# Performance work log

Hardware: AMD Instinct MI355X
Metric: run time of the kernel (lower is better)

The kernel has to match this reference:

```python
import jax, jax.numpy as jnp
import numpy as np


def setup_inputs() -> dict:
    key = jax.random.key(0)
    k1, k2 = jax.random.split(key)
    B, S, D, T = 64, 512, 768, 384
    hidden_states = jax.random.normal(k1, (B, S, D), dtype=jnp.float32)
    # sorted per-row segment ids: each subtoken belongs to a token index in [0, T)
    segment_ids = jnp.sort(jax.random.randint(k2, (B, S), 0, T), axis=-1)
    return {"hidden_states": hidden_states, "segment_ids": segment_ids, "num_tokens": T}


def reference(hidden_states, segment_ids, num_tokens):
    # Segment-mean of subtoken embeddings into token embeddings.
    # Equivalent to the original running-mean loop:
    #   prev + (next - prev) / n_subtoken_per_token  == mean over the group.
    B, S, D = hidden_states.shape
    # flatten batch into segment ids so one segment_sum handles all sequences
    flat_ids = (segment_ids + jnp.arange(B, dtype=segment_ids.dtype)[:, None] * num_tokens).reshape(-1)
    sums = jax.ops.segment_sum(hidden_states.reshape(-1, D), flat_ids,
                               num_segments=B * num_tokens)  # [B*T, D]
    counts = jax.ops.segment_sum(jnp.ones((B * S,), dtype=hidden_states.dtype), flat_ids,
                                 num_segments=B * num_tokens)  # [B*T]
    # tokens with no subtokens stay zero (original initializes with zeros)
    means = sums / jnp.maximum(counts, 1.0)[:, None]
    return means.reshape(B, num_tokens, D)
```

## Files before the change

### kernel.cpp

```cpp
#include <hip/hip_runtime.h>


__global__ void __launch_bounds__(192) seg_mean_kernel(
    const float* __restrict__ hs,
    const int* __restrict__ seg,
    const int* __restrict__ num_tokens_p,
    float* __restrict__ out,
    int BS_total,
    int D) {
  const int T = num_tokens_p[0];
  const int BT = gridDim.x;
  const int S = (int)(((long long)BS_total * T) / BT);
  const int b = blockIdx.x / T;
  const int t = blockIdx.x - b * T;

  const int* __restrict__ row = seg + (size_t)b * S;

  int lo = 0, n = S;
  while (n > 0) {
    int half = n >> 1;
    int mid = lo + half;
    if (row[mid] < t) { lo = mid + 1; n -= half + 1; } else { n = half; }
  }
  int hi = lo; n = S - lo;
  while (n > 0) {
    int half = n >> 1;
    int mid = hi + half;
    if (row[mid] < t + 1) { hi = mid + 1; n -= half + 1; } else { n = half; }
  }
  const int cnt = hi - lo;

  const int d4 = threadIdx.x;
  const int rowstride4 = D >> 2;

  const float4* __restrict__ p =
      (const float4*)(hs + ((size_t)b * S + lo) * D) + d4;

  float4 acc = make_float4(0.f, 0.f, 0.f, 0.f);
  for (int s = 0; s < cnt; ++s) {
    float4 v = p[(size_t)s * rowstride4];
    acc.x += v.x; acc.y += v.y; acc.z += v.z; acc.w += v.w;
  }

  const float inv = (cnt > 0) ? (1.0f / (float)cnt) : 0.0f;
  float4 o = make_float4(acc.x * inv, acc.y * inv, acc.z * inv, acc.w * inv);

  ((float4*)(out + (size_t)blockIdx.x * D))[d4] = o;
}

extern "C" void kernel_launch(void* const* d_in, const int* in_sizes, int n_in,
                              void* d_out, int out_size, void* d_ws, size_t ws_size,
                              hipStream_t stream) {
  const float* hs = (const float*)d_in[0];
  const int* seg = (const int*)d_in[1];
  const int* num_tokens_p = (const int*)d_in[2];
  float* out = (float*)d_out;

  const int BS_total = in_sizes[1];
  const int D = in_sizes[0] / in_sizes[1];
  const int BT = out_size / D;

  dim3 grid(BT);
  dim3 block(D / 4);
  hipLaunchKernelGGL(seg_mean_kernel, grid, block, 0, stream,
                     hs, seg, num_tokens_p, out, BS_total, D);
}
```

Measured before the change: 181.1 us.

## Precompute per-token segment start offsets in a separate kernel instead of binary search

Adds a preliminary kernel that scans the sorted segment ids and writes a per-row table of token start offsets into workspace. The mean kernel then reads its start and end from this table instead of running two dependent binary searches over the segment row. This removes the serial global-memory load chains at block start, at the cost of an extra launch and a workspace dependency. The old search-based kernel is kept as a fallback when workspace is too small.

```diff
diff --git a/kernel.cpp b/kernel.cpp
--- a/kernel.cpp
+++ b/kernel.cpp
@@ -1,9 +1,30 @@
 #include <hip/hip_runtime.h>
 
 
+__global__ void bounds_kernel(const int* __restrict__ seg,
+                              const int* __restrict__ num_tokens_p,
+                              int* __restrict__ start,
+                              int BS_total,
+                              int BT) {
+  const int T = num_tokens_p[0];
+  const int B = BT / T;
+  const int S = BS_total / B;
+  int idx = blockIdx.x * blockDim.x + threadIdx.x;
+  if (idx >= BS_total) return;
+  const int b = idx / S;
+  const int s = idx - b * S;
+  const int cur = seg[idx];
+  const int prev = (s == 0) ? -1 : seg[idx - 1];
+  int* __restrict__ row = start + (size_t)b * (T + 1);
+  for (int t = prev + 1; t <= cur; ++t) row[t] = s;
+  if (s == S - 1) {
+    for (int t = cur + 1; t <= T; ++t) row[t] = S;
+  }
+}
+
 __global__ void __launch_bounds__(192) seg_mean_kernel(
     const float* __restrict__ hs,
-    const int* __restrict__ seg,
+    const int* __restrict__ start,
     const int* __restrict__ num_tokens_p,
     float* __restrict__ out,
     int BS_total,
@@ -14,20 +35,9 @@
   const int b = blockIdx.x / T;
   const int t = blockIdx.x - b * T;
 
-  const int* __restrict__ row = seg + (size_t)b * S;
-
-  int lo = 0, n = S;
-  while (n > 0) {
-    int half = n >> 1;
-    int mid = lo + half;
-    if (row[mid] < t) { lo = mid + 1; n -= half + 1; } else { n = half; }
-  }
-  int hi = lo; n = S - lo;
-  while (n > 0) {
-    int half = n >> 1;
-    int mid = hi + half;
-    if (row[mid] < t + 1) { hi = mid + 1; n -= half + 1; } else { n = half; }
-  }
+  const int* __restrict__ srow = start + (size_t)b * (T + 1) + t;
+  const int lo = srow[0];
+  const int hi = srow[1];
   const int cnt = hi - lo;
 
   const int d4 = threadIdx.x;
@@ -48,6 +58,49 @@
   ((float4*)(out + (size_t)blockIdx.x * D))[d4] = o;
 }
 
+__global__ void __launch_bounds__(192) seg_mean_search_kernel(
+    const float* __restrict__ hs,
+    const int* __restrict__ seg,
+    const int* __restrict__ num_tokens_p,
+    float* __restrict__ out,
+    int BS_total,
+    int D) {
+  const int T = num_tokens_p[0];
+  const int BT = gridDim.x;
+  const int S = (int)(((long long)BS_total * T) / BT);
+  const int b = blockIdx.x / T;
+  const int t = blockIdx.x - b * T;
+  const int* __restrict__ row = seg + (size_t)b * S;
+
+  int lo = 0, n = S;
+  while (n > 0) {
+    int half = n >> 1;
+    int mid = lo + half;
+    if (row[mid] < t) { lo = mid + 1; n -= half + 1; } else { n = half; }
+  }
+  int hi = lo; n = S - lo;
+  while (n > 0) {
+    int half = n >> 1;
+    int mid = hi + half;
+    if (row[mid] < t + 1) { hi = mid + 1; n -= half + 1; } else { n = half; }
+  }
+  const int cnt = hi - lo;
+
+  const int d4 = threadIdx.x;
+  const int rowstride4 = D >> 2;
+  const float4* __restrict__ p =
+      (const float4*)(hs + ((size_t)b * S + lo) * D) + d4;
+
+  float4 acc = make_float4(0.f, 0.f, 0.f, 0.f);
+  for (int s = 0; s < cnt; ++s) {
+    float4 v = p[(size_t)s * rowstride4];
+    acc.x += v.x; acc.y += v.y; acc.z += v.z; acc.w += v.w;
+  }
+  const float inv = (cnt > 0) ? (1.0f / (float)cnt) : 0.0f;
+  float4 o = make_float4(acc.x * inv, acc.y * inv, acc.z * inv, acc.w * inv);
+  ((float4*)(out + (size_t)blockIdx.x * D))[d4] = o;
+}
+
 extern "C" void kernel_launch(void* const* d_in, const int* in_sizes, int n_in,
                               void* d_out, int out_size, void* d_ws, size_t ws_size,
                               hipStream_t stream) {
@@ -60,8 +113,18 @@
   const int D = in_sizes[0] / in_sizes[1];
   const int BT = out_size / D;
 
-  dim3 grid(BT);
-  dim3 block(D / 4);
-  hipLaunchKernelGGL(seg_mean_kernel, grid, block, 0, stream,
-                     hs, seg, num_tokens_p, out, BS_total, D);
+  const size_t ws_needed = (size_t)4 * ((size_t)BT + (size_t)BS_total);
+
+  if (ws_size >= ws_needed) {
+    int* start = (int*)d_ws;
+    const int threads1 = 256;
+    const int grid1 = (BS_total + threads1 - 1) / threads1;
+    hipLaunchKernelGGL(bounds_kernel, dim3(grid1), dim3(threads1), 0, stream,
+                       seg, num_tokens_p, start, BS_total, BT);
+    hipLaunchKernelGGL(seg_mean_kernel, dim3(BT), dim3(D / 4), 0, stream,
+                       hs, start, num_tokens_p, out, BS_total, D);
+  } else {
+    hipLaunchKernelGGL(seg_mean_search_kernel, dim3(BT), dim3(D / 4), 0, stream,
+                       hs, seg, num_tokens_p, out, BS_total, D);
+  }
 }
```

After: 174.7 us. -3.5%, faster.

## Precompute segment boundary table and process several tokens per wavefront

Applied to the files above, without the earlier changes.

Adds a first kernel that scatters segment start offsets into a workspace table, replacing the per-block binary searches over segment ids. The main kernel then assigns four consecutive tokens to each 64-lane wavefront, with each lane accumulating several float4 chunks in registers. This removes the search latency and the 192-thread blocks. In exchange it adds a second kernel launch and fewer, longer-running waves, which may lower memory-level parallelism for a bandwidth-bound read of about 100MB.

```diff
diff --git a/kernel.cpp b/kernel.cpp
--- a/kernel.cpp
+++ b/kernel.cpp
@@ -1,51 +1,88 @@
 #include <hip/hip_runtime.h>
 
 
-__global__ void __launch_bounds__(192) seg_mean_kernel(
+#define TPW 4
+#define WPB 4
+#define TPB (TPW * WPB)
+
+__global__ void table_kernel(const int* __restrict__ seg,
+                             const int* __restrict__ num_tokens_p,
+                             int* __restrict__ table,
+                             int BS_total,
+                             int BT) {
+  const int T = num_tokens_p[0];
+  const int B = BT / T;
+  const int S = BS_total / B;
+  int s = blockIdx.x * blockDim.x + threadIdx.x;
+  if (s >= BS_total) return;
+  const int b = s / S;
+  const int cur = b * T + seg[s];
+  const int prev = (s == 0) ? -1 : ((s - 1) / S) * T + seg[s - 1];
+  for (int g = prev + 1; g <= cur; ++g) table[g] = s;
+  if (s == BS_total - 1) {
+    for (int g = cur + 1; g <= BT; ++g) table[g] = BS_total;
+  }
+}
+
+template <int NCH>
+__global__ __launch_bounds__(WPB * 64) void seg_mean_kernel(
     const float* __restrict__ hs,
-    const int* __restrict__ seg,
-    const int* __restrict__ num_tokens_p,
+    const int* __restrict__ table,
     float* __restrict__ out,
-    int BS_total,
-    int D) {
-  const int T = num_tokens_p[0];
-  const int BT = gridDim.x;
-  const int S = (int)(((long long)BS_total * T) / BT);
-  const int b = blockIdx.x / T;
-  const int t = blockIdx.x - b * T;
+    int BT,
+    int D4) {
+  const int lane = threadIdx.x & 63;
+  const int wid = threadIdx.x >> 6;
+  const int g0 = (blockIdx.x * WPB + wid) * TPW;
+  if (g0 >= BT) return;
+  const int n = min(TPW, BT - g0);
 
-  const int* __restrict__ row = seg + (size_t)b * S;
+  int bnd[TPW + 1];
+#pragma unroll
+  for (int i = 0; i <= TPW; ++i) bnd[i] = (i <= n) ? table[g0 + i] : 0;
 
-  int lo = 0, n = S;
-  while (n > 0) {
-    int half = n >> 1;
-    int mid = lo + half;
-    if (row[mid] < t) { lo = mid + 1; n -= half + 1; } else { n = half; }
+  const float4* __restrict__ hs4 = (const float4*)hs;
+  float4* __restrict__ out4 = (float4*)out;
+
+  int r = bnd[0];
+  for (int tok = 0; tok < n; ++tok) {
+    const int rend = bnd[tok + 1];
+    float4 acc[NCH];
+#pragma unroll
+    for (int c = 0; c < NCH; ++c) acc[c] = make_float4(0.f, 0.f, 0.f, 0.f);
+    for (; r < rend; ++r) {
+      const float4* __restrict__ p = hs4 + (size_t)r * D4 + lane;
+#pragma unroll
+      for (int c = 0; c < NCH; ++c) {
+        float4 v = p[c * 64];
+        acc[c].x += v.x; acc[c].y += v.y; acc[c].z += v.z; acc[c].w += v.w;
+      }
+    }
+    const int cnt = rend - bnd[tok];
+    const float inv = (cnt > 0) ? (1.0f / (float)cnt) : 0.0f;
+    float4* __restrict__ q = out4 + (size_t)(g0 + tok) * D4 + lane;
+#pragma unroll
+    for (int c = 0; c < NCH; ++c) {
+      q[c * 64] = make_float4(acc[c].x * inv, acc[c].y * inv,
+                              acc[c].z * inv, acc[c].w * inv);
+    }
   }
-  int hi = lo; n = S - lo;
-  while (n > 0) {
-    int half = n >> 1;
-    int mid = hi + half;
-    if (row[mid] < t + 1) { hi = mid + 1; n -= half + 1; } else { n = half; }
+}
+
+__global__ void seg_mean_fallback(const float* __restrict__ hs,
+                                  const int* __restrict__ table,
+                                  float* __restrict__ out,
+                                  int D) {
+  const int g = blockIdx.x;
+  const int lo = table[g];
+  const int hi = table[g + 1];
+  const int cnt = hi - lo;
+  const float inv = (cnt > 0) ? (1.0f / (float)cnt) : 0.0f;
+  for (int d = threadIdx.x; d < D; d += blockDim.x) {
+    float a = 0.f;
+    for (int r = lo; r < hi; ++r) a += hs[(size_t)r * D + d];
+    out[(size_t)g * D + d] = a * inv;
   }
-  const int cnt = hi - lo;
-
-  const int d4 = threadIdx.x;
-  const int rowstride4 = D >> 2;
-
-  const float4* __restrict__ p =
-      (const float4*)(hs + ((size_t)b * S + lo) * D) + d4;
-
-  float4 acc = make_float4(0.f, 0.f, 0.f, 0.f);
-  for (int s = 0; s < cnt; ++s) {
-    float4 v = p[(size_t)s * rowstride4];
-    acc.x += v.x; acc.y += v.y; acc.z += v.z; acc.w += v.w;
-  }
-
-  const float inv = (cnt > 0) ? (1.0f / (float)cnt) : 0.0f;
-  float4 o = make_float4(acc.x * inv, acc.y * inv, acc.z * inv, acc.w * inv);
-
-  ((float4*)(out + (size_t)blockIdx.x * D))[d4] = o;
 }
 
 extern "C" void kernel_launch(void* const* d_in, const int* in_sizes, int n_in,
@@ -60,8 +97,36 @@
   const int D = in_sizes[0] / in_sizes[1];
   const int BT = out_size / D;
 
-  dim3 grid(BT);
-  dim3 block(D / 4);
-  hipLaunchKernelGGL(seg_mean_kernel, grid, block, 0, stream,
-                     hs, seg, num_tokens_p, out, BS_total, D);
+  int* table = (int*)d_ws;
+
+  const int threads1 = 256;
+  const int grid1 = (BS_total + threads1 - 1) / threads1;
+  hipLaunchKernelGGL(table_kernel, dim3(grid1), dim3(threads1), 0, stream,
+                     seg, num_tokens_p, table, BS_total, BT);
+
+  const int D4 = D / 4;
+  const int grid2 = (BT + TPB - 1) / TPB;
+  if (D % 4 == 0 && D4 % 64 == 0 && D4 / 64 >= 1 && D4 / 64 <= 4) {
+    switch (D4 / 64) {
+      case 1:
+        hipLaunchKernelGGL(seg_mean_kernel<1>, dim3(grid2), dim3(WPB * 64), 0,
+                           stream, hs, table, out, BT, D4);
+        break;
+      case 2:
+        hipLaunchKernelGGL(seg_mean_kernel<2>, dim3(grid2), dim3(WPB * 64), 0,
+                           stream, hs, table, out, BT, D4);
+        break;
+      case 3:
+        hipLaunchKernelGGL(seg_mean_kernel<3>, dim3(grid2), dim3(WPB * 64), 0,
+                           stream, hs, table, out, BT, D4);
+        break;
+      default:
+        hipLaunchKernelGGL(seg_mean_kernel<4>, dim3(grid2), dim3(WPB * 64), 0,
+                           stream, hs, table, out, BT, D4);
+        break;
+    }
+  } else {
+    hipLaunchKernelGGL(seg_mean_fallback, dim3(BT), dim3(256), 0, stream,
+                       hs, table, out, D);
+  }
 }
```

Result: no change. 179.9 us (-0.7%).
